# Performance work log

Hardware: AMD Instinct MI355X
Metric: run time of the kernel (lower is better)

## Reference

```python
import jax, jax.numpy as jnp
import numpy as np

B, T, D = 8, 1024, 1024
KD, VD, H = 1024, 1024, 16  # key_dim_total, value_dim_total, num_heads
NEG = -1e9
EPS = 1e-5


def setup_inputs() -> dict:
    key = jax.random.key(0)
    ks = jax.random.split(key, 8)
    x = jax.random.normal(ks[0], (B, T, D), dtype=jnp.float32)
    x_lens = jax.random.randint(ks[1], (B,), 1, T + 1).astype(jnp.int32)
    ln_gamma = jnp.ones((D,), jnp.float32)
    ln_beta = jnp.zeros((D,), jnp.float32)
    qkv_out = 2 * KD + VD
    w_qkv = jax.random.normal(ks[2], (D, qkv_out), jnp.float32) / np.sqrt(D)
    b_qkv = jax.random.normal(ks[3], (qkv_out,), jnp.float32) * 0.01
    w_out = jax.random.normal(ks[4], (VD, D), jnp.float32) / np.sqrt(VD)
    b_out = jax.random.normal(ks[5], (D,), jnp.float32) * 0.01
    return {"x": x, "x_lens": x_lens, "ln_gamma": ln_gamma, "ln_beta": ln_beta,
            "w_qkv": w_qkv, "b_qkv": b_qkv, "w_out": w_out, "b_out": b_out}


def reference(x, x_lens, ln_gamma, ln_beta, w_qkv, b_qkv, w_out, b_out):
    # LayerNorm over feature dim
    mu = jnp.mean(x, axis=-1, keepdims=True)
    var = jnp.mean(jnp.square(x - mu), axis=-1, keepdims=True)
    xn = (x - mu) * jax.lax.rsqrt(var + EPS) * ln_gamma + ln_beta
    # fused QKV projection
    qkv = xn @ w_qkv + b_qkv  # (B, T, 2*KD+VD)
    q, k, v = qkv[..., :KD], qkv[..., KD:2 * KD], qkv[..., 2 * KD:]
    hd = KD // H
    q = q.reshape(B, T, H, hd).transpose(0, 2, 1, 3)  # (B,H,T,hd)
    k = k.reshape(B, T, H, hd).transpose(0, 2, 1, 3)
    v = v.reshape(B, T, H, VD // H).transpose(0, 2, 1, 3)
    scale = 1.0 / np.sqrt(hd)
    scores = jnp.einsum("bhtd,bhsd->bhts", q, k) * scale  # (B,H,T,T)
    # combined causal + kv-length padding mask (additive in original; boolean here)
    causal = jnp.tril(jnp.ones((T, T), bool))  # (T,T)
    kv_valid = jnp.arange(T)[None, :] < x_lens[:, None]  # (B,T)
    mask = causal[None, None, :, :] & kv_valid[:, None, None, :]
    scores = jnp.where(mask, scores, NEG)
    att = jax.nn.softmax(scores, axis=-1)
    att_out = jnp.einsum("bhts,bhsd->bhtd", att, v)  # (B,H,T,hd_v)
    out = att_out.transpose(0, 2, 1, 3).reshape(B, T, VD)
    out = out @ w_out + b_out
    return out
```

## Files before the change

### kernel.cpp

```cpp
#include <hip/hip_runtime.h>

#define D_MODEL 1024
#define T_SEQ   1024
#define BATCH   8
#define NHEAD   16
#define HDIM    64

typedef float      v4f   __attribute__((ext_vector_type(4)));
typedef _Float16   half8 __attribute__((ext_vector_type(8)));
typedef _Float16   half4h __attribute__((ext_vector_type(4)));
typedef unsigned int ui4 __attribute__((ext_vector_type(4)));

__device__ __forceinline__ void load_lds16(const _Float16* g, _Float16* l) {
  __builtin_amdgcn_global_load_lds(
      (const __attribute__((address_space(1))) unsigned int*)g,
      (__attribute__((address_space(3))) unsigned int*)l, 16, 0, 0);
}

__global__ __launch_bounds__(256) void ln_kernel(const float* __restrict__ x,
                                                 const float* __restrict__ gamma,
                                                 const float* __restrict__ beta,
                                                 _Float16* __restrict__ xn) {
  int row = blockIdx.x;
  int tid = threadIdx.x;
  const float* xr = x + (size_t)row * D_MODEL;
  v4f xv = *(const v4f*)(xr + tid * 4);
  float s  = xv[0] + xv[1] + xv[2] + xv[3];
  float sq = xv[0]*xv[0] + xv[1]*xv[1] + xv[2]*xv[2] + xv[3]*xv[3];
#pragma unroll
  for (int off = 32; off > 0; off >>= 1) {
    s  += __shfl_xor(s, off);
    sq += __shfl_xor(sq, off);
  }
  __shared__ float ps[4], psq[4];
  int wave = tid >> 6;
  if ((tid & 63) == 0) { ps[wave] = s; psq[wave] = sq; }
  __syncthreads();
  float tot  = ps[0] + ps[1] + ps[2] + ps[3];
  float totq = psq[0] + psq[1] + psq[2] + psq[3];
  float mean = tot * (1.0f / D_MODEL);
  float var  = totq * (1.0f / D_MODEL) - mean * mean;
  float rs   = rsqrtf(var + 1e-5f);
  v4f gv = *(const v4f*)(gamma + tid * 4);
  v4f bv = *(const v4f*)(beta + tid * 4);
  half4h o;
#pragma unroll
  for (int i = 0; i < 4; ++i)
    o[i] = (_Float16)((xv[i] - mean) * rs * gv[i] + bv[i]);
  *(half4h*)(xn + (size_t)row * D_MODEL + tid * 4) = o;
}

__global__ __launch_bounds__(256) void fragize_kernel(const float* __restrict__ W,
                                                      _Float16* __restrict__ Bf,
                                                      int N, int K) {
  int g = blockIdx.x * 256 + threadIdx.x;
  int lane = g & 63, tile = g >> 6;
  int ktiles = K >> 5;
  int kt = tile % ktiles, nt = tile / ktiles;
  int n  = nt * 16 + (lane & 15);
  int k0 = kt * 32 + (lane >> 4) * 8;
  half8 o;
#pragma unroll
  for (int j = 0; j < 8; ++j) o[j] = (_Float16)W[(size_t)(k0 + j) * N + n];
  *(half8*)(Bf + (size_t)g * 8) = o;
}

__global__ __launch_bounds__(256) void vtrans_kernel(const _Float16* __restrict__ Vd,
                                                     _Float16* __restrict__ Vt) {
  __shared__ _Float16 tile[64][68];
  int p  = blockIdx.y;
  int t0 = blockIdx.x * 64;
  int tid = threadIdx.x;
  int r = tid >> 3, c = (tid & 7) * 8;
#pragma unroll
  for (int it = 0; it < 2; ++it) {
    int rr = r + it * 32;
    *(ui4*)&tile[rr][c] = *(const ui4*)&Vd[((size_t)p * T_SEQ + t0 + rr) * HDIM + c];
  }
  __syncthreads();
#pragma unroll
  for (int it = 0; it < 2; ++it) {
    int d = r + it * 32;
    half8 o;
#pragma unroll
    for (int j = 0; j < 8; ++j) o[j] = tile[c + j][d];
    *(half8*)&Vt[((size_t)p * HDIM + d) * T_SEQ + t0 + c] = o;
  }
}

template <int MODE>
__global__ __launch_bounds__(256) void gemm_kernel(
    const _Float16* __restrict__ A, const _Float16* __restrict__ Bfrag,
    const float* __restrict__ bias, int M, int N, int K,
    float* __restrict__ outF,
    _Float16* __restrict__ Qd, _Float16* __restrict__ Kd, _Float16* __restrict__ Vd) {
  __shared__ _Float16 As[3][4096];
  int tid = threadIdx.x;
  int wave = tid >> 6, lane = tid & 63;
  int l15 = lane & 15, quad = lane >> 4;
  int wm = (wave & 1) * 64, wn = (wave >> 1) * 64;
  int lin = blockIdx.y * gridDim.x + blockIdx.x;
  int xcd = lin & 7, idx = lin >> 3;
  int nmc = gridDim.x >> 3;
  int m0 = (xcd * nmc + (idx % nmc)) * 128;
  int n0 = (idx / nmc) * 128;
  v4f zero = {0.f, 0.f, 0.f, 0.f};
  v4f acc[4][4];
#pragma unroll
  for (int i = 0; i < 4; ++i)
#pragma unroll
    for (int j = 0; j < 4; ++j) acc[i][j] = zero;

  int ar0 = tid >> 2;
  int akc = (tid & 3) * 8;
  const _Float16* Ap = A + (size_t)(m0 + ar0) * K + akc;
  const int ktiles = K >> 5;
  const _Float16* Bp = Bfrag + (size_t)((n0 + wn) >> 4) * ktiles * 512 + lane * 8;

  {
    _Float16* w0 = &As[0][0] + wave * 512;
    load_lds16(Ap,                  w0);
    load_lds16(Ap + (size_t)64 * K, w0 + 2048);
    _Float16* w1 = &As[1][0] + wave * 512;
    load_lds16(Ap + 32,                  w1);
    load_lds16(Ap + 32 + (size_t)64 * K, w1 + 2048);
  }

  int cur = 0;
  for (int kt = 0; kt < ktiles; ++kt) {
    if (kt + 1 < ktiles) {
      asm volatile("s_waitcnt vmcnt(2)" ::: "memory");
    } else {
      asm volatile("s_waitcnt vmcnt(0)" ::: "memory");
    }
    __builtin_amdgcn_s_barrier();
    __builtin_amdgcn_sched_barrier(0);
    half8 bf[4];
#pragma unroll
    for (int ni = 0; ni < 4; ++ni)
      bf[ni] = *(const half8*)(Bp + ((size_t)ni * ktiles + kt) * 512);
    __builtin_amdgcn_sched_barrier(0);
    if (kt + 2 < ktiles) {
      int stg = cur == 0 ? 2 : cur - 1;
      _Float16* nx = &As[stg][0] + wave * 512;
      load_lds16(Ap + (kt + 2) * 32,                  nx);
      load_lds16(Ap + (kt + 2) * 32 + (size_t)64 * K, nx + 2048);
    }
    __builtin_amdgcn_sched_barrier(0);
    half8 af[4];
#pragma unroll
    for (int i = 0; i < 4; ++i)
      af[i] = *(const half8*)&As[cur][(wm + i * 16 + l15) * 32 + quad * 8];
#pragma unroll
    for (int mi = 0; mi < 4; ++mi)
#pragma unroll
      for (int ni = 0; ni < 4; ++ni)
        acc[mi][ni] = __builtin_amdgcn_mfma_f32_16x16x32_f16(af[mi], bf[ni], acc[mi][ni], 0, 0, 0);
    cur = cur == 2 ? 0 : cur + 1;
  }
  float bv[4];
#pragma unroll
  for (int ni = 0; ni < 4; ++ni) bv[ni] = bias[n0 + wn + ni * 16 + l15];
#pragma unroll
  for (int mi = 0; mi < 4; ++mi) {
#pragma unroll
    for (int ni = 0; ni < 4; ++ni) {
      int n = n0 + wn + ni * 16 + l15;
#pragma unroll
      for (int r = 0; r < 4; ++r) {
        int m = m0 + wm + mi * 16 + quad * 4 + r;
        float v = acc[mi][ni][r] + bv[ni];
        if (MODE == 1) {
          outF[(size_t)m * N + n] = v;
        } else {
          int b = m >> 10, t = m & 1023;
          int h = (n >> 6) & 15, d = n & 63;
          size_t idx2 = ((size_t)(b * NHEAD + h) * T_SEQ + t) * HDIM + d;
          if (n < 1024)        Qd[idx2] = (_Float16)(v * 0.18033688f);
          else if (n < 2048)   Kd[idx2] = (_Float16)v;
          else                 Vd[idx2] = (_Float16)v;
        }
      }
    }
  }
}

__global__ __launch_bounds__(256) void attn_kernel(const _Float16* __restrict__ Qg,
                                                   const _Float16* __restrict__ Kk,
                                                   const _Float16* __restrict__ Vt,
                                                   const int* __restrict__ x_lens,
                                                   _Float16* __restrict__ att) {
  __shared__ _Float16 Ks[2][2][2048];
  __shared__ _Float16 Vs[2][2][2048];
  __shared__ _Float16 Pb[4][16 * 72];
  int blk = blockIdx.x;
  int qt = 15 - (blk >> 7);
  int bh = blk & 127;
  int h  = bh & 15;
  int b  = bh >> 4;
  int t0 = qt * 64;
  int len = x_lens[b];
  int tid = threadIdx.x;
  int wave = tid >> 6, lane = tid & 63;
  int l15 = lane & 15, quad = lane >> 4;
  size_t plane = (size_t)(b * NHEAD + h) * (T_SEQ * HDIM);
  int qrow = t0 + wave * 16;
  int qabs = qrow + l15;
  const _Float16* Qp = Qg + plane + (size_t)qabs * HDIM + quad * 8;
  half8 qf0 = *(const half8*)Qp;
  half8 qf1 = *(const half8*)(Qp + 32);
  v4f zero = {0.f, 0.f, 0.f, 0.f};
  float m_i = -1e30f, l_i = 0.f;
  v4f Ov[4];
#pragma unroll
  for (int nt = 0; nt < 4; ++nt) Ov[nt] = zero;

  int jmaxb = min(t0 + 63, len - 1);
  int ntile = (jmaxb >> 6) + 1;
  int wjmax = min(qrow + 15, len - 1);

  const _Float16* src[4];
  _Float16* dst0[4];
  int strd[4];
#pragma unroll
  for (int i = 0; i < 4; ++i) {
    int u = wave * 4 + i;
    int q = u & 3, hf = (u >> 2) & 1;
    if (u < 8) {
      src[i] = Kk + plane + (size_t)(q * 16 + (lane >> 2)) * HDIM + hf * 32 + (lane & 3) * 8;
      dst0[i] = &Ks[0][hf][0] + q * 512;
      strd[i] = 64 * HDIM;
    } else {
      src[i] = Vt + plane + (size_t)(q * 16 + (lane >> 2)) * T_SEQ + hf * 32 + (lane & 3) * 8;
      dst0[i] = &Vs[0][hf][0] + q * 512;
      strd[i] = 64;
    }
  }

#pragma unroll
  for (int i = 0; i < 4; ++i) { load_lds16(src[i], dst0[i]); src[i] += strd[i]; }

  for (int jt = 0; jt < ntile; ++jt) {
    int j0 = jt * 64;
    int cur = jt & 1;
    __builtin_amdgcn_s_barrier();
    if (jt + 1 < ntile) {
#pragma unroll
      for (int i = 0; i < 4; ++i) {
        load_lds16(src[i], dst0[i] + (cur ^ 1) * 4096);
        src[i] += strd[i];
      }
      asm volatile("s_waitcnt vmcnt(4)" ::: "memory");
    } else {
      asm volatile("s_waitcnt vmcnt(0)" ::: "memory");
    }
    __builtin_amdgcn_s_barrier();
    __builtin_amdgcn_sched_barrier(0);
    if (j0 <= wjmax) {
      v4f s[4];
      __builtin_amdgcn_s_setprio(1);
#pragma unroll
      for (int nt = 0; nt < 4; ++nt) {
        s[nt] = zero;
        half8 k0 = *(const half8*)&Ks[cur][0][(nt * 16 + l15) * 32 + quad * 8];
        half8 k1 = *(const half8*)&Ks[cur][1][(nt * 16 + l15) * 32 + quad * 8];
        s[nt] = __builtin_amdgcn_mfma_f32_16x16x32_f16(k0, qf0, s[nt], 0, 0, 0);
        s[nt] = __builtin_amdgcn_mfma_f32_16x16x32_f16(k1, qf1, s[nt], 0, 0, 0);
      }
      __builtin_amdgcn_s_setprio(0);
      float mnew = m_i;
      bool full = (j0 + 63 <= qrow) && (j0 + 63 < len);
      if (full) {
#pragma unroll
        for (int nt = 0; nt < 4; ++nt)
#pragma unroll
          for (int r = 0; r < 4; ++r)
            mnew = fmaxf(mnew, s[nt][r]);
      } else {
#pragma unroll
        for (int nt = 0; nt < 4; ++nt) {
#pragma unroll
          for (int r = 0; r < 4; ++r) {
            int key = j0 + nt * 16 + quad * 4 + r;
            float v = (key <= qabs && key < len) ? s[nt][r] : -1e30f;
            s[nt][r] = v;
            mnew = fmaxf(mnew, v);
          }
        }
      }
      mnew = fmaxf(mnew, __shfl_xor(mnew, 16));
      mnew = fmaxf(mnew, __shfl_xor(mnew, 32));
      float alpha = exp2f(m_i - mnew);
      m_i = mnew;
      float rsum = 0.f;
#pragma unroll
      for (int nt = 0; nt < 4; ++nt)
#pragma unroll
        for (int r = 0; r < 4; ++r) {
          float p = exp2f(s[nt][r] - mnew);
          s[nt][r] = p;
          rsum += p;
        }
      rsum += __shfl_xor(rsum, 16);
      rsum += __shfl_xor(rsum, 32);
      l_i = l_i * alpha + rsum;
#pragma unroll
      for (int nt = 0; nt < 4; ++nt)
#pragma unroll
        for (int r = 0; r < 4; ++r) Ov[nt][r] *= alpha;
#pragma unroll
      for (int nt = 0; nt < 4; ++nt) {
        half4h pk;
#pragma unroll
        for (int r = 0; r < 4; ++r) pk[r] = (_Float16)s[nt][r];
        *(half4h*)&Pb[wave][l15 * 72 + nt * 16 + quad * 4] = pk;
      }
      asm volatile("s_waitcnt lgkmcnt(0)" ::: "memory");
      half8 pf0 = *(const half8*)&Pb[wave][l15 * 72 + quad * 8];
      half8 pf1 = *(const half8*)&Pb[wave][l15 * 72 + 32 + quad * 8];
      __builtin_amdgcn_s_setprio(1);
#pragma unroll
      for (int nt = 0; nt < 4; ++nt) {
        half8 v0 = *(const half8*)&Vs[cur][0][(nt * 16 + l15) * 32 + quad * 8];
        half8 v1 = *(const half8*)&Vs[cur][1][(nt * 16 + l15) * 32 + quad * 8];
        Ov[nt] = __builtin_amdgcn_mfma_f32_16x16x32_f16(v0, pf0, Ov[nt], 0, 0, 0);
        Ov[nt] = __builtin_amdgcn_mfma_f32_16x16x32_f16(v1, pf1, Ov[nt], 0, 0, 0);
      }
      __builtin_amdgcn_s_setprio(0);
    }
  }
  float inv = 1.0f / l_i;
#pragma unroll
  for (int nt = 0; nt < 4; ++nt) {
    half4h ok;
#pragma unroll
    for (int r = 0; r < 4; ++r) ok[r] = (_Float16)(Ov[nt][r] * inv);
    *(half4h*)&Pb[wave][l15 * 72 + nt * 16 + quad * 4] = ok;
  }
  asm volatile("s_waitcnt lgkmcnt(0)" ::: "memory");
  int r0 = lane >> 3, c0 = (lane & 7) * 8;
  half8 o0 = *(const half8*)&Pb[wave][r0 * 72 + c0];
  half8 o1 = *(const half8*)&Pb[wave][(r0 + 8) * 72 + c0];
  *(half8*)&att[((size_t)(b * T_SEQ) + qrow + r0) * D_MODEL + h * HDIM + c0] = o0;
  *(half8*)&att[((size_t)(b * T_SEQ) + qrow + r0 + 8) * D_MODEL + h * HDIM + c0] = o1;
}

extern "C" void kernel_launch(void* const* d_in, const int* in_sizes, int n_in,
                              void* d_out, int out_size, void* d_ws, size_t ws_size,
                              hipStream_t stream) {
  const float* x        = (const float*)d_in[0];
  const int*   x_lens   = (const int*)d_in[1];
  const float* ln_gamma = (const float*)d_in[2];
  const float* ln_beta  = (const float*)d_in[3];
  const float* w_qkv    = (const float*)d_in[4];
  const float* b_qkv    = (const float*)d_in[5];
  const float* w_out    = (const float*)d_in[6];
  const float* b_out    = (const float*)d_in[7];
  float* out = (float*)d_out;

  char* w = (char*)d_ws;
  _Float16* xn    = (_Float16*)w; w += (size_t)8192 * 1024 * 2;
  _Float16* BfQKV = (_Float16*)w; w += (size_t)3072 * 1024 * 2;
  _Float16* BfOut = (_Float16*)w; w += (size_t)1024 * 1024 * 2;
  _Float16* Qd    = (_Float16*)w; w += (size_t)8192 * 1024 * 2;
  _Float16* Kd    = (_Float16*)w; w += (size_t)8192 * 1024 * 2;
  _Float16* Vd    = (_Float16*)w; w += (size_t)8192 * 1024 * 2;
  _Float16* att   = (_Float16*)w; w += (size_t)8192 * 1024 * 2;
  _Float16* Vt    = xn;

  fragize_kernel<<<(3072 * 1024 / 8) / 256, 256, 0, stream>>>(w_qkv, BfQKV, 3072, 1024);
  fragize_kernel<<<(1024 * 1024 / 8) / 256, 256, 0, stream>>>(w_out, BfOut, 1024, 1024);
  ln_kernel<<<8192, 256, 0, stream>>>(x, ln_gamma, ln_beta, xn);
  gemm_kernel<0><<<dim3(8192 / 128, 3072 / 128), 256, 0, stream>>>(
      xn, BfQKV, b_qkv, 8192, 3072, 1024, nullptr, Qd, Kd, Vd);
  vtrans_kernel<<<dim3(16, 128), 256, 0, stream>>>(Vd, Vt);
  attn_kernel<<<2048, 256, 0, stream>>>(Qd, Kd, Vt, x_lens, att);
  gemm_kernel<1><<<dim3(8192 / 128, 1024 / 128), 256, 0, stream>>>(
      att, BfOut, b_out, 8192, 1024, 1024, out, nullptr, nullptr, nullptr);
}
```

Before: 247.8 us.

## Prefetch GEMM B fragments one k-step ahead and double attention query tile per block

The GEMM main loop is unrolled by two with ping-pong register buffers, so B fragments for the next k-tile are loaded from global memory while the current tile's MFMAs run. This hides B-load latency at the cost of extra registers. The attention kernel now runs 512 threads (8 waves) per block covering 128 query rows, so each K/V tile loaded to LDS is shared by twice as many waves and each wave issues half as many loads. The trade-off is coarser causal work balance and fewer blocks.

```diff
diff --git a/kernel.cpp b/kernel.cpp
--- a/kernel.cpp
+++ b/kernel.cpp
@@ -117,6 +117,34 @@
   const int ktiles = K >> 5;
   const _Float16* Bp = Bfrag + (size_t)((n0 + wn) >> 4) * ktiles * 512 + lane * 8;
 
+#define GPHASE(BFUSE, BFLD, KLD, BUFR, BUFS, KST, VN)                            \
+  {                                                                              \
+    asm volatile("s_waitcnt vmcnt(" #VN ")" ::: "memory");                       \
+    __builtin_amdgcn_s_barrier();                                                \
+    if ((KLD) >= 0) {                                                            \
+      _Pragma("unroll")                                                          \
+      for (int ni = 0; ni < 4; ++ni)                                             \
+        BFLD[ni] = *(const half8*)(Bp + ((size_t)ni * ktiles + (KLD)) * 512);    \
+    }                                                                            \
+    __builtin_amdgcn_sched_barrier(0);                                           \
+    if ((KST) >= 0) {                                                            \
+      _Float16* nx = &As[BUFS][0] + wave * 512;                                  \
+      load_lds16(Ap + (KST) * 32,                  nx);                          \
+      load_lds16(Ap + (KST) * 32 + (size_t)64 * K, nx + 2048);                   \
+    }                                                                            \
+    __builtin_amdgcn_sched_barrier(0);                                           \
+    half8 af[4];                                                                 \
+    _Pragma("unroll")                                                            \
+    for (int i = 0; i < 4; ++i)                                                  \
+      af[i] = *(const half8*)&As[BUFR][(wm + i * 16 + l15) * 32 + quad * 8];     \
+    _Pragma("unroll")                                                            \
+    for (int mi = 0; mi < 4; ++mi)                                               \
+      _Pragma("unroll")                                                          \
+      for (int ni = 0; ni < 4; ++ni)                                             \
+        acc[mi][ni] = __builtin_amdgcn_mfma_f32_16x16x32_f16(af[mi], BFUSE[ni],  \
+                                                             acc[mi][ni], 0,0,0);\
+  }
+
   {
     _Float16* w0 = &As[0][0] + wave * 512;
     load_lds16(Ap,                  w0);
@@ -125,39 +153,29 @@
     load_lds16(Ap + 32,                  w1);
     load_lds16(Ap + 32 + (size_t)64 * K, w1 + 2048);
   }
+  half8 bfA[4], bfB[4];
+#pragma unroll
+  for (int ni = 0; ni < 4; ++ni)
+    bfA[ni] = *(const half8*)(Bp + ((size_t)ni * ktiles) * 512);
 
   int cur = 0;
-  for (int kt = 0; kt < ktiles; ++kt) {
-    if (kt + 1 < ktiles) {
-      asm volatile("s_waitcnt vmcnt(2)" ::: "memory");
-    } else {
-      asm volatile("s_waitcnt vmcnt(0)" ::: "memory");
-    }
-    __builtin_amdgcn_s_barrier();
-    __builtin_amdgcn_sched_barrier(0);
-    half8 bf[4];
-#pragma unroll
-    for (int ni = 0; ni < 4; ++ni)
-      bf[ni] = *(const half8*)(Bp + ((size_t)ni * ktiles + kt) * 512);
-    __builtin_amdgcn_sched_barrier(0);
-    if (kt + 2 < ktiles) {
-      int stg = cur == 0 ? 2 : cur - 1;
-      _Float16* nx = &As[stg][0] + wave * 512;
-      load_lds16(Ap + (kt + 2) * 32,                  nx);
-      load_lds16(Ap + (kt + 2) * 32 + (size_t)64 * K, nx + 2048);
-    }
-    __builtin_amdgcn_sched_barrier(0);
-    half8 af[4];
-#pragma unroll
-    for (int i = 0; i < 4; ++i)
-      af[i] = *(const half8*)&As[cur][(wm + i * 16 + l15) * 32 + quad * 8];
-#pragma unroll
-    for (int mi = 0; mi < 4; ++mi)
-#pragma unroll
-      for (int ni = 0; ni < 4; ++ni)
-        acc[mi][ni] = __builtin_amdgcn_mfma_f32_16x16x32_f16(af[mi], bf[ni], acc[mi][ni], 0, 0, 0);
-    cur = cur == 2 ? 0 : cur + 1;
-  }
+  const int pairs = (ktiles >> 1) - 1;
+#pragma unroll 1
+  for (int p = 0; p < pairs; ++p) {
+    int kt  = 2 * p;
+    int nxt  = cur == 2 ? 0 : cur + 1;
+    int stgA = nxt == 2 ? 0 : nxt + 1;
+    GPHASE(bfA, bfB, kt + 1, cur, stgA, kt + 2, 6);
+    GPHASE(bfB, bfA, kt + 2, nxt, cur, kt + 3, 6);
+    cur = stgA;
+  }
+  {
+    int nxt = cur == 2 ? 0 : cur + 1;
+    GPHASE(bfA, bfB, ktiles - 1, cur, -1, -1, 6);
+    GPHASE(bfB, bfB, -1, nxt, -1, -1, 4);
+  }
+#undef GPHASE
+
   float bv[4];
 #pragma unroll
   for (int ni = 0; ni < 4; ++ni) bv[ni] = bias[n0 + wn + ni * 16 + l15];
@@ -185,20 +203,20 @@
   }
 }
 
-__global__ __launch_bounds__(256) void attn_kernel(const _Float16* __restrict__ Qg,
+__global__ __launch_bounds__(512) void attn_kernel(const _Float16* __restrict__ Qg,
                                                    const _Float16* __restrict__ Kk,
                                                    const _Float16* __restrict__ Vt,
                                                    const int* __restrict__ x_lens,
                                                    _Float16* __restrict__ att) {
   __shared__ _Float16 Ks[2][2][2048];
   __shared__ _Float16 Vs[2][2][2048];
-  __shared__ _Float16 Pb[4][16 * 72];
+  __shared__ _Float16 Pb[8][16 * 72];
   int blk = blockIdx.x;
-  int qt = 15 - (blk >> 7);
+  int qt = 7 - (blk >> 7);
   int bh = blk & 127;
   int h  = bh & 15;
   int b  = bh >> 4;
-  int t0 = qt * 64;
+  int t0 = qt * 128;
   int len = x_lens[b];
   int tid = threadIdx.x;
   int wave = tid >> 6, lane = tid & 63;
@@ -215,16 +233,16 @@
 #pragma unroll
   for (int nt = 0; nt < 4; ++nt) Ov[nt] = zero;
 
-  int jmaxb = min(t0 + 63, len - 1);
+  int jmaxb = min(t0 + 127, len - 1);
   int ntile = (jmaxb >> 6) + 1;
   int wjmax = min(qrow + 15, len - 1);
 
-  const _Float16* src[4];
-  _Float16* dst0[4];
-  int strd[4];
-#pragma unroll
-  for (int i = 0; i < 4; ++i) {
-    int u = wave * 4 + i;
+  const _Float16* src[2];
+  _Float16* dst0[2];
+  int strd[2];
+#pragma unroll
+  for (int i = 0; i < 2; ++i) {
+    int u = wave * 2 + i;
     int q = u & 3, hf = (u >> 2) & 1;
     if (u < 8) {
       src[i] = Kk + plane + (size_t)(q * 16 + (lane >> 2)) * HDIM + hf * 32 + (lane & 3) * 8;
@@ -238,7 +256,7 @@
   }
 
 #pragma unroll
-  for (int i = 0; i < 4; ++i) { load_lds16(src[i], dst0[i]); src[i] += strd[i]; }
+  for (int i = 0; i < 2; ++i) { load_lds16(src[i], dst0[i]); src[i] += strd[i]; }
 
   for (int jt = 0; jt < ntile; ++jt) {
     int j0 = jt * 64;
@@ -246,11 +264,11 @@
     __builtin_amdgcn_s_barrier();
     if (jt + 1 < ntile) {
 #pragma unroll
-      for (int i = 0; i < 4; ++i) {
+      for (int i = 0; i < 2; ++i) {
         load_lds16(src[i], dst0[i] + (cur ^ 1) * 4096);
         src[i] += strd[i];
       }
-      asm volatile("s_waitcnt vmcnt(4)" ::: "memory");
+      asm volatile("s_waitcnt vmcnt(2)" ::: "memory");
     } else {
       asm volatile("s_waitcnt vmcnt(0)" ::: "memory");
     }
@@ -374,7 +392,7 @@
   gemm_kernel<0><<<dim3(8192 / 128, 3072 / 128), 256, 0, stream>>>(
       xn, BfQKV, b_qkv, 8192, 3072, 1024, nullptr, Qd, Kd, Vd);
   vtrans_kernel<<<dim3(16, 128), 256, 0, stream>>>(Vd, Vt);
-  attn_kernel<<<2048, 256, 0, stream>>>(Qd, Kd, Vt, x_lens, att);
+  attn_kernel<<<1024, 512, 0, stream>>>(Qd, Kd, Vt, x_lens, att);
   gemm_kernel<1><<<dim3(8192 / 128, 1024 / 128), 256, 0, stream>>>(
       att, BfOut, b_out, 8192, 1024, 1024, out, nullptr, nullptr, nullptr);
 }
```

After: 242.6 us. 1.02x faster.
